# Kernel tuning notes

Hardware: AMD Instinct MI355X
Metric: run time of the kernel (lower is better)

The kernel has to match this reference:

```python
import jax, jax.numpy as jnp
import numpy as np

B, C, W, H = 4, 512, 64, 64
C8 = C // 8


def setup_inputs() -> dict:
    key = jax.random.key(0)
    ks = jax.random.split(key, 8)
    s = 1.0 / np.sqrt(C)  # conv2d 1x1 fan-in init scale
    return {
        "x": jax.random.normal(ks[0], (B, C, W, H), jnp.float32),
        "y": jax.random.normal(ks[1], (B, C, W, H), jnp.float32),
        "wq": jax.random.uniform(ks[2], (C8, C), jnp.float32, -s, s),
        "bq": jax.random.uniform(ks[3], (C8,), jnp.float32, -s, s),
        "wk": jax.random.uniform(ks[4], (C8, C), jnp.float32, -s, s),
        "bk": jax.random.uniform(ks[5], (C8,), jnp.float32, -s, s),
        "wv": jax.random.uniform(ks[6], (C, C), jnp.float32, -s, s),
        "bv": jax.random.uniform(ks[7], (C,), jnp.float32, -s, s),
        "gamma": jnp.zeros((1,), jnp.float32),
    }


def reference(x, y, wq, bq, wk, bk, wv, bv, gamma):
    b, c, w, h = x.shape
    n = w * h
    yf = y.reshape(b, c, n)        # [B, C, N]
    xf = x.reshape(b, c, n)        # [B, C, N]
    # 1x1 convs are channel-wise linear maps
    q = jnp.einsum('oc,bcn->bno', wq, yf) + bq              # [B, N, C8]
    k = jnp.einsum('oc,bcn->bon', wk, yf) + bk[:, None]      # [B, C8, N]
    energy = jnp.einsum('bno,bom->bnm', q, k)                # [B, N, N], no scaling (as in source)
    attention = jax.nn.softmax(energy, axis=2)
    v = jnp.einsum('oc,bcn->bon', wv, xf) + bv[:, None]      # [B, C, N]
    # out[b,c,m] = sum_n v[b,c,n] * attention[b,m,n]  (bmm with attention^T)
    out = jnp.einsum('bcn,bmn->bcm', v, attention).reshape(b, c, w, h)
    out = gamma[0] * out + x
    return (out, attention)
```

## Files before the change

kernel.cpp:

```cpp
#include <hip/hip_runtime.h>


#define BB 4
#define CC 512
#define NN 4096
#define C8V 64

typedef __bf16 bf16x8 __attribute__((ext_vector_type(8)));
typedef float f32x4 __attribute__((ext_vector_type(4)));
typedef float f32x4v __attribute__((ext_vector_type(4)));
typedef unsigned short u16x8 __attribute__((ext_vector_type(8)));

#if __has_builtin(__builtin_amdgcn_exp2f)
#define EXP2(x) __builtin_amdgcn_exp2f(x)
#else
#define EXP2(x) exp2f(x)
#endif

#define MFMA16(a, b, c) __builtin_amdgcn_mfma_f32_16x16x32_bf16((a), (b), (c), 0, 0, 0)

__device__ __forceinline__ unsigned short f2b(float f) {
  union { float f; unsigned u; } x; x.f = f;
  unsigned u = x.u;
  u += 0x7fffu + ((u >> 16) & 1u);
  return (unsigned short)(u >> 16);
}

__device__ __forceinline__ float b2f(unsigned short s) {
  union { unsigned u; float f; } x; x.u = ((unsigned)s) << 16;
  return x.f;
}

__device__ __forceinline__ bf16x8 ldb8(const unsigned short* p) {
  return *reinterpret_cast<const bf16x8*>(p);
}

__global__ __launch_bounds__(256) void k_cvt_w(
    const float* __restrict__ wq, const float* __restrict__ wk, const float* __restrict__ wv,
    unsigned short* __restrict__ wqb, unsigned short* __restrict__ wkb, unsigned short* __restrict__ wvb) {
  int i = blockIdx.x * 256 + threadIdx.x;
  if (i < 32768)        wqb[i] = f2b(wq[i]);
  else if (i < 65536)   wkb[i - 32768] = f2b(wk[i - 32768]);
  else if (i < 327680)  wvb[i - 65536] = f2b(wv[i - 65536]);
}

__global__ __launch_bounds__(256) void k_projqk(
    const float* __restrict__ y,
    const unsigned short* __restrict__ wqb, const unsigned short* __restrict__ wkb,
    const float* __restrict__ bq, const float* __restrict__ bk,
    unsigned short* __restrict__ q, unsigned short* __restrict__ ktp) {
  __shared__ unsigned short ytile[64][130];
  int b = blockIdx.y, n0 = blockIdx.x * 64;
  int t = threadIdx.x, w = t >> 6, l = t & 63, lr = l & 15, lk = l >> 4;
  const float* yb = y + (size_t)b * CC * NN;

  f32x4 qacc[4] = {}, kacc[4] = {};
  for (int slab = 0; slab < 4; slab++) {
    int cs = slab * 128;
#pragma unroll
    for (int r = 0; r < 8; r++) {
      int idx = t + r * 256, c = idx >> 4, n4 = (idx & 15) * 4;
      f32x4v v4 = *reinterpret_cast<const f32x4v*>(&yb[(size_t)(cs + c) * NN + n0 + n4]);
      ytile[n4 + 0][c] = f2b(v4.x); ytile[n4 + 1][c] = f2b(v4.y);
      ytile[n4 + 2][c] = f2b(v4.z); ytile[n4 + 3][c] = f2b(v4.w);
    }
    __syncthreads();
#pragma unroll
    for (int ks = 0; ks < 4; ks++) {
      bf16x8 a = *reinterpret_cast<const bf16x8*>(&ytile[w * 16 + lr][ks * 32 + lk * 8]);
      int cgl = cs + ks * 32 + lk * 8;
#pragma unroll
      for (int cg = 0; cg < 4; cg++) {
        qacc[cg] = MFMA16(a, ldb8(wqb + (size_t)(cg * 16 + lr) * CC + cgl), qacc[cg]);
        kacc[cg] = MFMA16(a, ldb8(wkb + (size_t)(cg * 16 + lr) * CC + cgl), kacc[cg]);
      }
    }
    __syncthreads();
  }
#pragma unroll
  for (int cg = 0; cg < 4; cg++) {
    int o = cg * 16 + lr;
    float bqv = bq[o], bkv = bk[o];
#pragma unroll
    for (int i = 0; i < 4; i++) {
      int n = n0 + w * 16 + lk * 4 + i;
      q[(size_t)(b * NN + n) * C8V + o] = f2b((qacc[cg][i] + bqv) * 1.44269504088896f);
      ktp[((size_t)(b * 256 + (n >> 4)) * 2 + (o >> 5)) * 512 + (n & 15) * 32 + (o & 31)] =
          f2b(kacc[cg][i] + bkv);
    }
  }
}

__global__ __launch_bounds__(512) void k_projv(
    const float* __restrict__ x, const unsigned short* __restrict__ wvb,
    const float* __restrict__ bv, unsigned short* __restrict__ vp) {
  __shared__ unsigned short xtile[64][130];
  int b = blockIdx.y, n0 = blockIdx.x * 64;
  int t = threadIdx.x, w = t >> 6, l = t & 63, lr = l & 15, lk = l >> 4;
  const float* xb = x + (size_t)b * CC * NN;
  int c0w = w * 64;

  f32x4 acc[4][4] = {};
  for (int slab = 0; slab < 4; slab++) {
    int cs = slab * 128;
#pragma unroll
    for (int r = 0; r < 4; r++) {
      int idx = t + r * 512, c = idx >> 4, n4 = (idx & 15) * 4;
      f32x4v v4 = *reinterpret_cast<const f32x4v*>(&xb[(size_t)(cs + c) * NN + n0 + n4]);
      xtile[n4 + 0][c] = f2b(v4.x); xtile[n4 + 1][c] = f2b(v4.y);
      xtile[n4 + 2][c] = f2b(v4.z); xtile[n4 + 3][c] = f2b(v4.w);
    }
    __syncthreads();
#pragma unroll
    for (int ks = 0; ks < 4; ks++) {
      bf16x8 bfr[4];
#pragma unroll
      for (int cg = 0; cg < 4; cg++)
        bfr[cg] = *reinterpret_cast<const bf16x8*>(&xtile[cg * 16 + lr][ks * 32 + lk * 8]);
#pragma unroll
      for (int rg = 0; rg < 4; rg++) {
        bf16x8 a = ldb8(wvb + (size_t)(c0w + rg * 16 + lr) * CC + cs + ks * 32 + lk * 8);
#pragma unroll
        for (int cg = 0; cg < 4; cg++)
          acc[rg][cg] = MFMA16(a, bfr[cg], acc[rg][cg]);
      }
    }
    __syncthreads();
  }
#pragma unroll
  for (int rg = 0; rg < 4; rg++)
#pragma unroll
    for (int i = 0; i < 4; i++) {
      int c = c0w + rg * 16 + lk * 4 + i;
      float bias = bv[c];
#pragma unroll
      for (int cg = 0; cg < 4; cg++) {
        int n = n0 + cg * 16 + lr;
        vp[((size_t)(b * 64 + (n >> 6)) * 2 + ((n >> 5) & 1)) * 16384 + c * 32 + (n & 31)] =
            f2b(acc[rg][cg][i] + bias);
      }
    }
}

__global__ __launch_bounds__(512, 2) void k_fused(const unsigned short* __restrict__ q,
                                                  const unsigned short* __restrict__ ktp,
                                                  const unsigned short* __restrict__ vp,
                                                  const float* __restrict__ x,
                                                  const float* __restrict__ gamma,
                                                  float* __restrict__ out,
                                                  float* __restrict__ att) {
  __shared__ unsigned short smP[2][64 * 64];
  __shared__ float psum[8][16];

  int bid = blockIdx.x;
  int b = (bid & 7) >> 1;
  int m0 = ((bid >> 3) * 2 + (bid & 1)) * 64;
  int t = threadIdx.x, w = t >> 6, l = t & 63, lr = l & 15, lk = l >> 4;
  int rg = w >> 1, nh = w & 1;
  int c0w = w * 64;
  int mrow = t >> 3, col8 = t & 7;

  float* ab = att + (size_t)b * NN * NN;

  const unsigned short* qp = q + (size_t)(b * NN + m0 + rg * 16 + lr) * C8V + lk * 8;
  bf16x8 aq0 = ldb8(qp), aq1 = ldb8(qp + 32);

  float lsum[4] = {0.f, 0.f, 0.f, 0.f};
  for (int jt = 0; jt < 64; jt++) {
    f32x4 acc2[2] = {};
#pragma unroll
    for (int cg = 0; cg < 2; cg++) {
      size_t base = ((size_t)(b * 256 + jt * 4 + nh * 2 + cg) * 2) * 512 + lr * 32 + lk * 8;
      acc2[cg] = MFMA16(aq0, ldb8(ktp + base), acc2[cg]);
      acc2[cg] = MFMA16(aq1, ldb8(ktp + base + 512), acc2[cg]);
    }
#pragma unroll
    for (int i = 0; i < 4; i++)
      lsum[i] += EXP2(acc2[0][i]) + EXP2(acc2[1][i]);
  }
#pragma unroll
  for (int i = 0; i < 4; i++) {
#pragma unroll
    for (int mm = 1; mm < 16; mm <<= 1) lsum[i] += __shfl_xor(lsum[i], mm);
  }
  if (lr == 0) {
#pragma unroll
    for (int i = 0; i < 4; i++) psum[w][lk * 4 + i] = lsum[i];
  }
  __syncthreads();
  f32x4v invv;
#pragma unroll
  for (int i = 0; i < 4; i++)
    invv[i] = 1.0f / (psum[rg * 2][lk * 4 + i] + psum[rg * 2 + 1][lk * 4 + i]);

#define LDKT(D, JT)                                                            \
  _Pragma("unroll")                                                            \
  for (int cg = 0; cg < 2; cg++) {                                             \
    size_t base = ((size_t)(b * 256 + (JT) * 4 + nh * 2 + cg) * 2) * 512 +     \
                  lr * 32 + lk * 8;                                            \
    D[cg * 2] = ldb8(ktp + base);                                              \
    D[cg * 2 + 1] = ldb8(ktp + base + 512);                                    \
  }

#define LDV(D, JT)                                                             \
  _Pragma("unroll")                                                            \
  for (int rg2 = 0; rg2 < 4; rg2++) {                                          \
    size_t vbase = ((size_t)(b * 64 + (JT)) * 2) * 16384 +                     \
                   (c0w + rg2 * 16 + lr) * 32 + lk * 8;                        \
    D[rg2 * 2] = ldb8(vp + vbase);                                             \
    D[rg2 * 2 + 1] = ldb8(vp + vbase + 16384);                                 \
  }

#define QKSM(KT, BUF)                                                          \
  {                                                                            \
    char* pbuf = reinterpret_cast<char*>(&smP[BUF][0]);                        \
    _Pragma("unroll")                                                          \
    for (int cg = 0; cg < 2; cg++) {                                           \
      f32x4 z = {};                                                            \
      z = MFMA16(aq0, KT[cg * 2], z);                                          \
      z = MFMA16(aq1, KT[cg * 2 + 1], z);                                      \
      int nl = nh * 32 + cg * 16 + lr;                                         \
      _Pragma("unroll")                                                        \
      for (int i = 0; i < 4; i++) {                                            \
        int ml = rg * 16 + lk * 4 + i;                                         \
        float p = EXP2(z[i]) * invv[i];                                        \
        *reinterpret_cast<unsigned short*>(                                    \
            pbuf + ml * 128 + ((nl * 2) ^ ((ml & 7) << 4))) = f2b(p);          \
      }                                                                        \
    }                                                                          \
  }

#define ATTST(BUF, JT)                                                         \
  {                                                                            \
    const char* pr = reinterpret_cast<const char*>(&smP[BUF][0]);              \
    u16x8 raw = *reinterpret_cast<const u16x8*>(                               \
        pr + mrow * 128 + ((col8 * 16) ^ ((mrow & 7) << 4)));                  \
    f32x4v lo, hi;                                                             \
    lo.x = b2f(raw[0]); lo.y = b2f(raw[1]); lo.z = b2f(raw[2]);                \
    lo.w = b2f(raw[3]); hi.x = b2f(raw[4]); hi.y = b2f(raw[5]);                \
    hi.z = b2f(raw[6]); hi.w = b2f(raw[7]);                                    \
    float* dst = &ab[(size_t)(m0 + mrow) * NN + (JT) * 64 + col8 * 8];         \
    *reinterpret_cast<f32x4v*>(dst) = lo;                                      \
    *reinterpret_cast<f32x4v*>(dst + 4) = hi;                                  \
  }

#define PV(VR, BUF)                                                            \
  {                                                                            \
    const char* pr = reinterpret_cast<const char*>(&smP[BUF][0]);              \
    __builtin_amdgcn_s_setprio(1);                                             \
    _Pragma("unroll")                                                          \
    for (int ks = 0; ks < 2; ks++) {                                           \
      bf16x8 bfr[4];                                                           \
      _Pragma("unroll")                                                        \
      for (int cg = 0; cg < 4; cg++) {                                         \
        int mr = cg * 16 + lr;                                                 \
        bfr[cg] = *reinterpret_cast<const bf16x8*>(                            \
            pr + mr * 128 + ((ks * 64 + lk * 16) ^ ((mr & 7) << 4)));          \
      }                                                                        \
      _Pragma("unroll")                                                        \
      for (int rg2 = 0; rg2 < 4; rg2++)                                        \
        _Pragma("unroll")                                                      \
        for (int cg = 0; cg < 4; cg++)                                         \
          acc[rg2][cg] = MFMA16(VR[rg2 * 2 + ks], bfr[cg], acc[rg2][cg]);      \
    }                                                                          \
    __builtin_amdgcn_s_setprio(0);                                             \
  }

#define SB() __builtin_amdgcn_sched_barrier(0);

#define SYNC_NODRAIN()                                   \
  asm volatile("s_waitcnt lgkmcnt(0)" ::: "memory");     \
  __builtin_amdgcn_s_barrier();                          \
  __builtin_amdgcn_sched_barrier(0);

  f32x4 acc[4][4] = {};
  bf16x8 ktA[4], ktB[4];
  bf16x8 vA[8], vB[8];

  LDKT(ktA, 0);
  LDV(vA, 0);
  QKSM(ktA, 0);
  LDKT(ktB, 1);
  SYNC_NODRAIN();

#define BODY(G, KTF, VN, KTC, VC, CUR)                                         \
  {                                                                            \
    int g = (G);                                                               \
    if (g < 62) LDKT(KTF, g + 2);                             \
    if (g < 63) LDV(VN, g + 1);                                                \
    SB();                                                                      \
    ATTST(CUR, g);                                     \
    SB();                                                                      \
    if (g < 63) QKSM(KTC, (CUR) ^ 1);                \
    PV(VC, CUR);                                                               \
    SYNC_NODRAIN();                                                            \
  }

  for (int g2 = 0; g2 < 64; g2 += 2) {
    BODY(g2,     ktA, vB, ktB, vA, 0);
    BODY(g2 + 1, ktB, vA, ktA, vB, 1);
  }
#undef LDKT
#undef LDV
#undef QKSM
#undef ATTST
#undef PV
#undef SB
#undef SYNC_NODRAIN
#undef BODY

  float gm = gamma[0];
  const float* xb = x + (size_t)b * CC * NN;
  float* ob = out + (size_t)b * CC * NN;
#pragma unroll
  for (int rg2 = 0; rg2 < 4; rg2++)
#pragma unroll
    for (int i = 0; i < 4; i++) {
      int row = c0w + rg2 * 16 + lk * 4 + i;
#pragma unroll
      for (int cg = 0; cg < 4; cg++) {
        int col = m0 + cg * 16 + lr;
        size_t off = (size_t)row * NN + col;
        float xv = __builtin_nontemporal_load(&xb[off]);
        ob[off] = gm * acc[rg2][cg][i] + xv;
      }
    }
}

extern "C" void kernel_launch(void* const* d_in, const int* in_sizes, int n_in,
                              void* d_out, int out_size, void* d_ws, size_t ws_size,
                              hipStream_t stream) {
  const float* x  = (const float*)d_in[0];
  const float* y  = (const float*)d_in[1];
  const float* wq = (const float*)d_in[2];
  const float* bq = (const float*)d_in[3];
  const float* wk = (const float*)d_in[4];
  const float* bk = (const float*)d_in[5];
  const float* wv = (const float*)d_in[6];
  const float* bv = (const float*)d_in[7];
  const float* gamma = (const float*)d_in[8];

  float* out = (float*)d_out;
  float* att = out + (size_t)BB * CC * NN;

  char* ws = (char*)d_ws;
  unsigned short* q   = (unsigned short*)(ws);
  unsigned short* ktp = (unsigned short*)(ws + 2097152);
  unsigned short* vp  = (unsigned short*)(ws + 4194304);
  unsigned short* wqb = (unsigned short*)(ws + 20971520);
  unsigned short* wkb = (unsigned short*)(ws + 21037056);
  unsigned short* wvb = (unsigned short*)(ws + 21102592);
  if (ws_size < 21626880u) return;

  k_cvt_w<<<1280, 256, 0, stream>>>(wq, wk, wv, wqb, wkb, wvb);
  k_projqk<<<dim3(64, 4), 256, 0, stream>>>(y, wqb, wkb, bq, bk, q, ktp);
  k_projv<<<dim3(64, 4), 512, 0, stream>>>(x, wvb, bv, vp);
  k_fused<<<256, 512, 0, stream>>>(q, ktp, vp, x, gamma, out, att);
}
```

Measured before the change: 257.6 us.

## Halve query tile per block, specialize waves for QK-softmax vs attention stores

Each block now handles 32 query rows instead of 64, and the grid doubles to 512 blocks with a launch bound of 4 blocks per CU. The row-sum pass is redistributed so every wave covers a strided subset of key tiles for both 16-row groups, and the partial sums are reduced through shared memory. Within the main loop, waves 0-3 compute QK and the softmax tile while waves 4-7 write the fp32 attention tile, so those two jobs run on separate waves. This aims to raise occupancy and overlap, but it doubles total V streaming relative to the work done and halves the MFMA reuse of each V fragment.

```diff
diff --git a/kernel.cpp b/kernel.cpp
--- a/kernel.cpp
+++ b/kernel.cpp
@@ -142,56 +142,75 @@
     }
 }
 
-__global__ __launch_bounds__(512, 2) void k_fused(const unsigned short* __restrict__ q,
+__global__ __launch_bounds__(512, 4) void k_fused(const unsigned short* __restrict__ q,
                                                   const unsigned short* __restrict__ ktp,
                                                   const unsigned short* __restrict__ vp,
                                                   const float* __restrict__ x,
                                                   const float* __restrict__ gamma,
                                                   float* __restrict__ out,
                                                   float* __restrict__ att) {
-  __shared__ unsigned short smP[2][64 * 64];
-  __shared__ float psum[8][16];
+  __shared__ unsigned short smP[2][32 * 64];
+  __shared__ float psum[8][32];
 
   int bid = blockIdx.x;
   int b = (bid & 7) >> 1;
-  int m0 = ((bid >> 3) * 2 + (bid & 1)) * 64;
+  int m0 = ((bid >> 3) * 2 + (bid & 1)) * 32;
   int t = threadIdx.x, w = t >> 6, l = t & 63, lr = l & 15, lk = l >> 4;
-  int rg = w >> 1, nh = w & 1;
+  int rg = w & 1, nh = (w >> 1) & 1;
   int c0w = w * 64;
-  int mrow = t >> 3, col8 = t & 7;
+  int ti = (t - 256) & 255;
+  int mrow = ti >> 3, col8 = ti & 7;
 
   float* ab = att + (size_t)b * NN * NN;
 
-  const unsigned short* qp = q + (size_t)(b * NN + m0 + rg * 16 + lr) * C8V + lk * 8;
-  bf16x8 aq0 = ldb8(qp), aq1 = ldb8(qp + 32);
-
-  float lsum[4] = {0.f, 0.f, 0.f, 0.f};
-  for (int jt = 0; jt < 64; jt++) {
-    f32x4 acc2[2] = {};
-#pragma unroll
-    for (int cg = 0; cg < 2; cg++) {
-      size_t base = ((size_t)(b * 256 + jt * 4 + nh * 2 + cg) * 2) * 512 + lr * 32 + lk * 8;
-      acc2[cg] = MFMA16(aq0, ldb8(ktp + base), acc2[cg]);
-      acc2[cg] = MFMA16(aq1, ldb8(ktp + base + 512), acc2[cg]);
-    }
-#pragma unroll
-    for (int i = 0; i < 4; i++)
-      lsum[i] += EXP2(acc2[0][i]) + EXP2(acc2[1][i]);
-  }
-#pragma unroll
-  for (int i = 0; i < 4; i++) {
-#pragma unroll
-    for (int mm = 1; mm < 16; mm <<= 1) lsum[i] += __shfl_xor(lsum[i], mm);
-  }
+  bf16x8 qf[2][2];
+#pragma unroll
+  for (int rgp = 0; rgp < 2; rgp++) {
+    const unsigned short* qp = q + (size_t)(b * NN + m0 + rgp * 16 + lr) * C8V + lk * 8;
+    qf[rgp][0] = ldb8(qp);
+    qf[rgp][1] = ldb8(qp + 32);
+  }
+
+  float lsum[2][4] = {};
+  for (int jc = 0; jc < 8; jc++) {
+    int jt = w + jc * 8;
+#pragma unroll
+    for (int cg = 0; cg < 4; cg++) {
+      size_t base = ((size_t)(b * 256 + jt * 4 + cg) * 2) * 512 + lr * 32 + lk * 8;
+      bf16x8 k0 = ldb8(ktp + base), k1 = ldb8(ktp + base + 512);
+#pragma unroll
+      for (int rgp = 0; rgp < 2; rgp++) {
+        f32x4 z = {};
+        z = MFMA16(qf[rgp][0], k0, z);
+        z = MFMA16(qf[rgp][1], k1, z);
+#pragma unroll
+        for (int i = 0; i < 4; i++) lsum[rgp][i] += EXP2(z[i]);
+      }
+    }
+  }
+#pragma unroll
+  for (int rgp = 0; rgp < 2; rgp++)
+#pragma unroll
+    for (int i = 0; i < 4; i++) {
+#pragma unroll
+      for (int mm = 1; mm < 16; mm <<= 1) lsum[rgp][i] += __shfl_xor(lsum[rgp][i], mm);
+    }
   if (lr == 0) {
 #pragma unroll
-    for (int i = 0; i < 4; i++) psum[w][lk * 4 + i] = lsum[i];
+    for (int rgp = 0; rgp < 2; rgp++)
+#pragma unroll
+      for (int i = 0; i < 4; i++) psum[w][rgp * 16 + lk * 4 + i] = lsum[rgp][i];
   }
   __syncthreads();
   f32x4v invv;
 #pragma unroll
-  for (int i = 0; i < 4; i++)
-    invv[i] = 1.0f / (psum[rg * 2][lk * 4 + i] + psum[rg * 2 + 1][lk * 4 + i]);
+  for (int i = 0; i < 4; i++) {
+    int r = rg * 16 + lk * 4 + i;
+    float s = 0.f;
+#pragma unroll
+    for (int ww = 0; ww < 8; ww++) s += psum[ww][r];
+    invv[i] = 1.0f / s;
+  }
 
 #define LDKT(D, JT)                                                            \
   _Pragma("unroll")                                                            \
@@ -217,8 +236,8 @@
     _Pragma("unroll")                                                          \
     for (int cg = 0; cg < 2; cg++) {                                           \
       f32x4 z = {};                                                            \
-      z = MFMA16(aq0, KT[cg * 2], z);                                          \
-      z = MFMA16(aq1, KT[cg * 2 + 1], z);                                      \
+      z = MFMA16(qf[rg][0], KT[cg * 2], z);                                    \
+      z = MFMA16(qf[rg][1], KT[cg * 2 + 1], z);                                \
       int nl = nh * 32 + cg * 16 + lr;                                         \
       _Pragma("unroll")                                                        \
       for (int i = 0; i < 4; i++) {                                            \
@@ -250,9 +269,9 @@
     __builtin_amdgcn_s_setprio(1);                                             \
     _Pragma("unroll")                                                          \
     for (int ks = 0; ks < 2; ks++) {                                           \
-      bf16x8 bfr[4];                                                           \
+      bf16x8 bfr[2];                                                           \
       _Pragma("unroll")                                                        \
-      for (int cg = 0; cg < 4; cg++) {                                         \
+      for (int cg = 0; cg < 2; cg++) {                                         \
         int mr = cg * 16 + lr;                                                 \
         bfr[cg] = *reinterpret_cast<const bf16x8*>(                            \
             pr + mr * 128 + ((ks * 64 + lk * 16) ^ ((mr & 7) << 4)));          \
@@ -260,7 +279,7 @@
       _Pragma("unroll")                                                        \
       for (int rg2 = 0; rg2 < 4; rg2++)                                        \
         _Pragma("unroll")                                                      \
-        for (int cg = 0; cg < 4; cg++)                                         \
+        for (int cg = 0; cg < 2; cg++)                                         \
           acc[rg2][cg] = MFMA16(VR[rg2 * 2 + ks], bfr[cg], acc[rg2][cg]);      \
     }                                                                          \
     __builtin_amdgcn_s_setprio(0);                                             \
@@ -273,25 +292,33 @@
   __builtin_amdgcn_s_barrier();                          \
   __builtin_amdgcn_sched_barrier(0);
 
-  f32x4 acc[4][4] = {};
+  f32x4 acc[4][2] = {};
   bf16x8 ktA[4], ktB[4];
   bf16x8 vA[8], vB[8];
 
-  LDKT(ktA, 0);
+  if (w < 4) {
+    LDKT(ktA, 0);
+  }
   LDV(vA, 0);
-  QKSM(ktA, 0);
-  LDKT(ktB, 1);
+  if (w < 4) {
+    QKSM(ktA, 0);
+    LDKT(ktB, 1);
+  }
   SYNC_NODRAIN();
 
 #define BODY(G, KTF, VN, KTC, VC, CUR)                                         \
   {                                                                            \
     int g = (G);                                                               \
-    if (g < 62) LDKT(KTF, g + 2);                             \
+    if (w < 4) {                                                               \
+      if (g < 62) LDKT(KTF, g + 2);                           \
+    }                                                                          \
     if (g < 63) LDV(VN, g + 1);                                                \
     SB();                                                                      \
-    ATTST(CUR, g);                                     \
+    if (w >= 4) ATTST(CUR, g);                         \
     SB();                                                                      \
-    if (g < 63) QKSM(KTC, (CUR) ^ 1);                \
+    if (w < 4) {                                                               \
+      if (g < 63) QKSM(KTC, (CUR) ^ 1);              \
+    }                                                                          \
     PV(VC, CUR);                                                               \
     SYNC_NODRAIN();                                                            \
   }
@@ -318,7 +345,7 @@
     for (int i = 0; i < 4; i++) {
       int row = c0w + rg2 * 16 + lk * 4 + i;
 #pragma unroll
-      for (int cg = 0; cg < 4; cg++) {
+      for (int cg = 0; cg < 2; cg++) {
         int col = m0 + cg * 16 + lr;
         size_t off = (size_t)row * NN + col;
         float xv = __builtin_nontemporal_load(&xb[off]);
@@ -355,5 +382,5 @@
   k_cvt_w<<<1280, 256, 0, stream>>>(wq, wk, wv, wqb, wkb, wvb);
   k_projqk<<<dim3(64, 4), 256, 0, stream>>>(y, wqb, wkb, bq, bk, q, ktp);
   k_projv<<<dim3(64, 4), 512, 0, stream>>>(x, wvb, bv, vp);
-  k_fused<<<256, 512, 0, stream>>>(q, ktp, vp, x, gamma, out, att);
-}
+  k_fused<<<512, 512, 0, stream>>>(q, ktp, vp, x, gamma, out, att);
+}
```

Result: slower. 783.1 us (+204.1%).

## Process two key tiles per barrier with four-deep LDS probability buffers

Applied to the files above, without the earlier changes.

The fused attention loop now handles two 64-column tiles per iteration. It uses four shared-memory P buffers instead of two, so barriers per tile are halved and there is more independent work between syncs. The K and V register prefetches are reordered: V loads for the next pair are issued after the PV MFMAs, and the priority boost now spans both PV blocks. The cost is double the LDS for P, which may reduce occupancy at 2 blocks/CU. It also exposes more V-load latency, since the V loads are issued late, after the MFMAs.

```diff
diff --git a/kernel.cpp b/kernel.cpp
--- a/kernel.cpp
+++ b/kernel.cpp
@@ -149,7 +149,7 @@
                                                   const float* __restrict__ gamma,
                                                   float* __restrict__ out,
                                                   float* __restrict__ att) {
-  __shared__ unsigned short smP[2][64 * 64];
+  __shared__ unsigned short smP[4][64 * 64];
   __shared__ float psum[8][16];
 
   int bid = blockIdx.x;
@@ -247,7 +247,6 @@
 #define PV(VR, BUF)                                                            \
   {                                                                            \
     const char* pr = reinterpret_cast<const char*>(&smP[BUF][0]);              \
-    __builtin_amdgcn_s_setprio(1);                                             \
     _Pragma("unroll")                                                          \
     for (int ks = 0; ks < 2; ks++) {                                           \
       bf16x8 bfr[4];                                                           \
@@ -263,7 +262,6 @@
         for (int cg = 0; cg < 4; cg++)                                         \
           acc[rg2][cg] = MFMA16(VR[rg2 * 2 + ks], bfr[cg], acc[rg2][cg]);      \
     }                                                                          \
-    __builtin_amdgcn_s_setprio(0);                                             \
   }
 
 #define SB() __builtin_amdgcn_sched_barrier(0);
@@ -278,27 +276,42 @@
   bf16x8 vA[8], vB[8];
 
   LDKT(ktA, 0);
+  LDKT(ktB, 1);
   LDV(vA, 0);
+  LDV(vB, 1);
   QKSM(ktA, 0);
-  LDKT(ktB, 1);
+  QKSM(ktB, 1);
+  LDKT(ktA, 2);
+  LDKT(ktB, 3);
   SYNC_NODRAIN();
 
-#define BODY(G, KTF, VN, KTC, VC, CUR)                                         \
+#define BODY2(G, B0, B1, B2, B3)                                               \
   {                                                                            \
     int g = (G);                                                               \
-    if (g < 62) LDKT(KTF, g + 2);                             \
-    if (g < 63) LDV(VN, g + 1);                                                \
+    ATTST(B0, g);                                                              \
+    ATTST(B1, g + 1);                                                          \
     SB();                                                                      \
-    ATTST(CUR, g);                                     \
+    if (g < 62) {                                                              \
+      QKSM(ktA, B2);                                  \
+      QKSM(ktB, B3);                                  \
+      LDKT(ktA, (g + 4 > 63 ? 63 : g + 4));                                    \
+      LDKT(ktB, (g + 5 > 63 ? 63 : g + 5));                                    \
+    }                                                                          \
     SB();                                                                      \
-    if (g < 63) QKSM(KTC, (CUR) ^ 1);                \
-    PV(VC, CUR);                                                               \
+    __builtin_amdgcn_s_setprio(1);                                             \
+    PV(vA, B0);                                                                \
+    PV(vB, B1);                                                                \
+    __builtin_amdgcn_s_setprio(0);                                             \
+    if (g < 62) {                                                              \
+      LDV(vA, g + 2);                                                          \
+      LDV(vB, g + 3);                                                          \
+    }                                                                          \
     SYNC_NODRAIN();                                                            \
   }
 
-  for (int g2 = 0; g2 < 64; g2 += 2) {
-    BODY(g2,     ktA, vB, ktB, vA, 0);
-    BODY(g2 + 1, ktB, vA, ktA, vB, 1);
+  for (int g4 = 0; g4 < 64; g4 += 4) {
+    BODY2(g4,     0, 1, 2, 3);
+    BODY2(g4 + 2, 2, 3, 0, 1);
   }
 #undef LDKT
 #undef LDV
@@ -307,7 +320,7 @@
 #undef PV
 #undef SB
 #undef SYNC_NODRAIN
-#undef BODY
+#undef BODY2
 
   float gm = gamma[0];
   const float* xb = x + (size_t)b * CC * NN;
```

Measured after the change: 260.5 us. Within noise of the previous version (+1.1%).
